# Optimization experiments

Measured on AMD Instinct MI355X. Metric: run time of the kernel, lower is better.

The kernel has to match this reference:

```python
import jax, jax.numpy as jnp
import numpy as np

N_NODES = 100000
D_EMB = 128          # per-node embedding dim; concat dim = 2*D_EMB = 256
HIDDEN = 64
N_EDGES = 300000


def setup_inputs() -> dict:
    key = jax.random.key(0)
    ks = jax.random.split(key, 8)
    src_embs = jax.random.normal(ks[0], (N_NODES, D_EMB), dtype=jnp.float32)
    dst_embs = jax.random.normal(ks[1], (N_NODES, D_EMB), dtype=jnp.float32)
    edges_src_ids = jax.random.randint(ks[2], (N_EDGES,), 0, N_NODES, dtype=jnp.int64)
    edges_dst_ids = jax.random.randint(ks[3], (N_EDGES,), 0, N_NODES, dtype=jnp.int64)
    # elayers = Linear(256, 64) -> ReLU -> Linear(64, 1)
    s1 = 1.0 / np.sqrt(2 * D_EMB)
    s2 = 1.0 / np.sqrt(HIDDEN)
    W1 = jax.random.uniform(ks[4], (2 * D_EMB, HIDDEN), jnp.float32, -s1, s1)
    b1 = jax.random.uniform(ks[5], (HIDDEN,), jnp.float32, -s1, s1)
    W2 = jax.random.uniform(ks[6], (HIDDEN, 1), jnp.float32, -s2, s2)
    b2 = jax.random.uniform(ks[7], (1,), jnp.float32, -s2, s2)
    return {
        "src_embs": src_embs,
        "dst_embs": dst_embs,
        "edges_src_ids": edges_src_ids,
        "edges_dst_ids": edges_dst_ids,
        "W1": W1,
        "b1": b1,
        "W2": W2,
        "b2": b2,
    }


def reference(src_embs, dst_embs, edges_src_ids, edges_dst_ids, W1, b1, W2, b2):
    # Gather per-edge endpoint embeddings and concatenate: [E, 2*D]
    edge_feats = jnp.concatenate(
        [src_embs[edges_src_ids], dst_embs[edges_dst_ids]], axis=1
    )
    # Linear -> ReLU -> Linear, producing one logit per edge: [E, 1]
    h = jax.nn.relu(edge_feats @ W1 + b1)
    edge_logits = h @ W2 + b2
    return edge_logits
```

## Files before the change

### kernel.cpp

```cpp
#include <hip/hip_runtime.h>
#include <hip/hip_bf16.h>

typedef float f32x4 __attribute__((ext_vector_type(4)));
typedef __bf16 bf16x8 __attribute__((ext_vector_type(8)));
typedef __bf16 bf16x4 __attribute__((ext_vector_type(4)));

#define DEMB 128
#define HIDDEN 64
#define W1T_STRIDE 264

typedef const __attribute__((address_space(1))) void* gas_ptr;
typedef __attribute__((address_space(3))) void* las_ptr;

__global__ __launch_bounds__(256) void node_part3_kernel(
    const float* __restrict__ src_embs,
    const float* __restrict__ dst_embs,
    const float* __restrict__ W1,
    __bf16* __restrict__ spart,
    __bf16* __restrict__ dpart,
    int n_tiles, int blocks_per_table)
{
    __shared__ __bf16 frag_lds[1024 * 8];
    __shared__ float  atile[4][2048];

    const int table = (blockIdx.x >= blocks_per_table) ? 1 : 0;
    const int bid = blockIdx.x - table * blocks_per_table;
    const float* __restrict__ E = table ? dst_embs : src_embs;
    __bf16* __restrict__ P = table ? dpart : spart;
    const int kofs = table * 128;

    for (int cid = threadIdx.x; cid < 1024; cid += 256) {
        const int el = cid & 15;
        const int gk = (cid >> 4) & 3;
        const int kk = (cid >> 6) & 3;
        const int t  = (cid >> 8) & 3;
        const int kbase = kofs + kk * 32 + gk * 8;
        bf16x8 ch;
#pragma unroll
        for (int j = 0; j < 8; ++j)
            ch[j] = (__bf16)W1[(kbase + j) * HIDDEN + 4 * el + t];
        *reinterpret_cast<bf16x8*>(&frag_lds[cid * 8]) = ch;
    }
    __syncthreads();

    const int lane = threadIdx.x & 63;
    const int el = lane & 15;
    const int gk = lane >> 4;
    const int wid = threadIdx.x >> 6;
    char* awc = (char*)&atile[wid][0];

    int soff[8];
#pragma unroll
    for (int op = 0; op < 8; ++op) {
        const int d = op * 1024 + lane * 16;
        soff[op] = d ^ (((d >> 9) & 7) << 4);
    }
    const int abase = (el * 512 + gk * 32) ^ ((el & 7) << 4);

    const int tstride = blocks_per_table * 4;
    for (int tile = bid * 4 + wid; tile < n_tiles; tile += tstride) {
        const char* ebase = (const char*)E + (size_t)tile * (16 * DEMB * 4);
#pragma unroll
        for (int op = 0; op < 8; ++op) {
            __builtin_amdgcn_global_load_lds(
                (gas_ptr)(ebase + soff[op]),
                (las_ptr)(awc + op * 1024), 16, 0, 0);
        }
        asm volatile("s_waitcnt vmcnt(0)" ::: "memory");

        f32x4 acc[4] = {{0.f,0.f,0.f,0.f},{0.f,0.f,0.f,0.f},
                        {0.f,0.f,0.f,0.f},{0.f,0.f,0.f,0.f}};
#pragma unroll
        for (int kk = 0; kk < 4; ++kk) {
            const int ab = abase + kk * 128;
            f32x4 lo = *reinterpret_cast<const f32x4*>(awc + ab);
            f32x4 hi = *reinterpret_cast<const f32x4*>(awc + (ab ^ 16));
            bf16x8 a;
#pragma unroll
            for (int j = 0; j < 4; ++j) { a[j] = (__bf16)lo[j]; a[4+j] = (__bf16)hi[j]; }
#pragma unroll
            for (int t = 0; t < 4; ++t) {
                const bf16x8 b = *reinterpret_cast<const bf16x8*>(
                    &frag_lds[(size_t)((t * 4 + kk) * 4 + gk) * 128 + el * 8]);
                acc[t] = __builtin_amdgcn_mfma_f32_16x16x32_bf16(a, b, acc[t], 0, 0, 0);
            }
        }

        asm volatile("" ::: "memory");
#pragma unroll
        for (int r = 0; r < 4; ++r) {
            bf16x4 pk;
#pragma unroll
            for (int t = 0; t < 4; ++t) pk[t] = (__bf16)acc[t][r];
            *reinterpret_cast<bf16x4*>(awc + (gk * 4 + r) * 128 + el * 8) = pk;
        }
        asm volatile("s_waitcnt lgkmcnt(0)" ::: "memory");
        f32x4 c0 = *reinterpret_cast<const f32x4*>(awc + lane * 32);
        f32x4 c1 = *reinterpret_cast<const f32x4*>(awc + lane * 32 + 16);
        char* pb = (char*)P + (size_t)tile * 2048;
        *reinterpret_cast<f32x4*>(pb + lane * 32) = c0;
        *reinterpret_cast<f32x4*>(pb + lane * 32 + 16) = c1;
    }
}

__global__ __launch_bounds__(256, 8) void edge_tail2_kernel(
    const __bf16* __restrict__ spart,
    const __bf16* __restrict__ dpart,
    const int* __restrict__ src_ids,
    const int* __restrict__ dst_ids,
    const float* __restrict__ b1,
    const float* __restrict__ W2,
    const float* __restrict__ b2,
    float* __restrict__ out,
    int n_edges)
{
    const int lane = threadIdx.x & 63;
    const int c = lane & 7;
    float b1v[8], w2v[8];
#pragma unroll
    for (int j = 0; j < 8; ++j) { b1v[j] = b1[c * 8 + j]; w2v[j] = W2[c * 8 + j]; }
    const float bias2 = b2[0];

    int gid = (blockIdx.x * blockDim.x + threadIdx.x) >> 3;
    const int gstride = (gridDim.x * blockDim.x) >> 3;

    for (int e = gid; e < n_edges; e += gstride) {
        const long long sid = src_ids[e];
        const long long did = dst_ids[e];
        const bf16x8 s8 = *reinterpret_cast<const bf16x8*>(spart + sid * HIDDEN + c * 8);
        const bf16x8 d8 = *reinterpret_cast<const bf16x8*>(dpart + did * HIDDEN + c * 8);
        float v = 0.f;
#pragma unroll
        for (int j = 0; j < 8; ++j) {
            float h = (float)s8[j] + (float)d8[j] + b1v[j];
            h = fmaxf(h, 0.f);
            v = fmaf(h, w2v[j], v);
        }
        v += __shfl_xor(v, 1, 64);
        v += __shfl_xor(v, 2, 64);
        v += __shfl_xor(v, 4, 64);
        if (c == 0) out[e] = v + bias2;
    }
}

__global__ __launch_bounds__(256) void edge_mlp_kernel(
    const float* __restrict__ src_embs,
    const float* __restrict__ dst_embs,
    const int* __restrict__ src_ids,
    const int* __restrict__ dst_ids,
    const float* __restrict__ W1,
    const float* __restrict__ b1,
    const float* __restrict__ W2,
    const float* __restrict__ b2,
    float* __restrict__ out,
    int n_edges, int n_groups)
{
    __shared__ __bf16 w1t[64 * W1T_STRIDE];
    for (int s = threadIdx.x; s < 256 * 64; s += 256) {
        int k = s >> 6;
        int n = s & 63;
        w1t[n * W1T_STRIDE + k] = (__bf16)W1[s];
    }
    __syncthreads();

    const int lane = threadIdx.x & 63;
    const int el = lane & 15;
    const int gk = lane >> 4;

    float b1v[4], w2v[4];
#pragma unroll
    for (int t = 0; t < 4; ++t) { b1v[t] = b1[16 * t + el]; w2v[t] = W2[16 * t + el]; }
    const float bias2 = b2[0];

    const int gw0 = blockIdx.x * 4 + (threadIdx.x >> 6);
    const int gstride = gridDim.x * 4;

    for (int g = gw0; g < n_groups; g += gstride) {
        const int e_base = g * 16;
        int e = e_base + el;
        if (e >= n_edges) e = n_edges - 1;
        const long long sid = src_ids[e];
        const long long did = dst_ids[e];
        const float* sp = src_embs + sid * DEMB + gk * 8;
        const float* dp = dst_embs + did * DEMB + gk * 8;

        f32x4 acc[4] = {{0.f,0.f,0.f,0.f},{0.f,0.f,0.f,0.f},
                        {0.f,0.f,0.f,0.f},{0.f,0.f,0.f,0.f}};
#pragma unroll
        for (int kk = 0; kk < 8; ++kk) {
            const float* ap = (kk < 4) ? (sp + kk * 32) : (dp + (kk - 4) * 32);
            f32x4 f0 = *reinterpret_cast<const f32x4*>(ap);
            f32x4 f1 = *reinterpret_cast<const f32x4*>(ap + 4);
            bf16x8 a;
#pragma unroll
            for (int j = 0; j < 4; ++j) { a[j] = (__bf16)f0[j]; a[4+j] = (__bf16)f1[j]; }
#pragma unroll
            for (int t = 0; t < 4; ++t) {
                const bf16x8 bfrag = *reinterpret_cast<const bf16x8*>(
                    &w1t[(16 * t + el) * W1T_STRIDE + kk * 32 + gk * 8]);
                acc[t] = __builtin_amdgcn_mfma_f32_16x16x32_bf16(a, bfrag, acc[t], 0, 0, 0);
            }
        }
        float s0[4];
#pragma unroll
        for (int r = 0; r < 4; ++r) {
            float v = 0.f;
#pragma unroll
            for (int t = 0; t < 4; ++t) {
                float h = acc[t][r] + b1v[t];
                h = fmaxf(h, 0.f);
                v = fmaf(h, w2v[t], v);
            }
#pragma unroll
            for (int m = 1; m < 16; m <<= 1) v += __shfl_xor(v, m, 64);
            s0[r] = v + bias2;
        }
        const int row0 = e_base + gk * 4;
        if (el == 0) {
            if (row0 + 4 <= n_edges) {
                f32x4 o = {s0[0], s0[1], s0[2], s0[3]};
                *reinterpret_cast<f32x4*>(out + row0) = o;
            } else {
#pragma unroll
                for (int r = 0; r < 4; ++r)
                    if (row0 + r < n_edges) out[row0 + r] = s0[r];
            }
        }
    }
}

extern "C" void kernel_launch(void* const* d_in, const int* in_sizes, int n_in,
                              void* d_out, int out_size, void* d_ws, size_t ws_size,
                              hipStream_t stream) {
    const float* src_embs = (const float*)d_in[0];
    const float* dst_embs = (const float*)d_in[1];
    const int*   src_ids  = (const int*)d_in[2];
    const int*   dst_ids  = (const int*)d_in[3];
    const float* W1 = (const float*)d_in[4];
    const float* b1 = (const float*)d_in[5];
    const float* W2 = (const float*)d_in[6];
    const float* b2 = (const float*)d_in[7];
    float* out = (float*)d_out;

    const int n_edges = in_sizes[2];
    const int n_nodes = in_sizes[0] / DEMB;
    const size_t part_elems = (size_t)n_nodes * HIDDEN;
    const size_t need = 2 * part_elems * sizeof(__bf16);

    if (ws_size >= need && (n_nodes % 16) == 0) {
        __bf16* spart = (__bf16*)d_ws;
        __bf16* dpart = spart + part_elems;
        const int n_tiles = n_nodes / 16;

        int bpt = 384;
        if (bpt * 4 > n_tiles) bpt = (n_tiles + 3) / 4;
        node_part3_kernel<<<2 * bpt, 256, 0, stream>>>(
            src_embs, dst_embs, W1, spart, dpart, n_tiles, bpt);

        int blocks2 = (n_edges + 31) / 32;
        if (blocks2 > 2048) blocks2 = 2048;
        edge_tail2_kernel<<<blocks2, 256, 0, stream>>>(
            spart, dpart, src_ids, dst_ids, b1, W2, b2, out, n_edges);
    } else {
        const int n_groups = (n_edges + 15) / 16;
        int blocks = (n_groups + 3) / 4;
        if (blocks > 1024) blocks = 1024;
        edge_mlp_kernel<<<blocks, 256, 0, stream>>>(
            src_embs, dst_embs, src_ids, dst_ids, W1, b1, W2, b2, out,
            n_edges, n_groups);
    }
}
```

Measured before the change: 40.37 us.

## Double-buffer node tile loads with prefetch in a 2-wave block

```diff
diff --git a/kernel.cpp b/kernel.cpp
--- a/kernel.cpp
+++ b/kernel.cpp
@@ -12,7 +12,7 @@
 typedef const __attribute__((address_space(1))) void* gas_ptr;
 typedef __attribute__((address_space(3))) void* las_ptr;
 
-__global__ __launch_bounds__(256) void node_part3_kernel(
+__global__ __launch_bounds__(128) void node_part4_kernel(
     const float* __restrict__ src_embs,
     const float* __restrict__ dst_embs,
     const float* __restrict__ W1,
@@ -21,7 +21,8 @@
     int n_tiles, int blocks_per_table)
 {
     __shared__ __bf16 frag_lds[1024 * 8];
-    __shared__ float  atile[4][2048];
+    __shared__ float  stage[2][2][2048];
+    __shared__ float  bounce[2][512];
 
     const int table = (blockIdx.x >= blocks_per_table) ? 1 : 0;
     const int bid = blockIdx.x - table * blocks_per_table;
@@ -29,7 +30,7 @@
     __bf16* __restrict__ P = table ? dpart : spart;
     const int kofs = table * 128;
 
-    for (int cid = threadIdx.x; cid < 1024; cid += 256) {
+    for (int cid = threadIdx.x; cid < 1024; cid += 128) {
         const int el = cid & 15;
         const int gk = (cid >> 4) & 3;
         const int kk = (cid >> 6) & 3;
@@ -47,7 +48,9 @@
     const int el = lane & 15;
     const int gk = lane >> 4;
     const int wid = threadIdx.x >> 6;
-    char* awc = (char*)&atile[wid][0];
+    char* buf0 = (char*)&stage[wid][0][0];
+    char* buf1 = (char*)&stage[wid][1][0];
+    char* obc  = (char*)&bounce[wid][0];
 
     int soff[8];
 #pragma unroll
@@ -57,16 +60,36 @@
     }
     const int abase = (el * 512 + gk * 32) ^ ((el & 7) << 4);
 
-    const int tstride = blocks_per_table * 4;
-    for (int tile = bid * 4 + wid; tile < n_tiles; tile += tstride) {
-        const char* ebase = (const char*)E + (size_t)tile * (16 * DEMB * 4);
-#pragma unroll
-        for (int op = 0; op < 8; ++op) {
-            __builtin_amdgcn_global_load_lds(
-                (gas_ptr)(ebase + soff[op]),
-                (las_ptr)(awc + op * 1024), 16, 0, 0);
-        }
-        asm volatile("s_waitcnt vmcnt(0)" ::: "memory");
+#define ISSUE_TILE(T, DST)                                                  \
+    do {                                                                    \
+        const char* eb_ = (const char*)E + (size_t)(T) * (16 * DEMB * 4);   \
+        _Pragma("unroll")                                                   \
+        for (int op = 0; op < 8; ++op)                                      \
+            __builtin_amdgcn_global_load_lds((gas_ptr)(eb_ + soff[op]),     \
+                                             (las_ptr)((DST) + op * 1024),  \
+                                             16, 0, 0);                     \
+    } while (0)
+
+    const int tstride = blocks_per_table * 2;
+    int tile = bid * 2 + wid;
+    int cur = 0;
+    bool have_stores = false;
+
+    if (tile < n_tiles) ISSUE_TILE(tile, buf0);
+
+    while (tile < n_tiles) {
+        const int nxt = tile + tstride;
+        const bool pf = (nxt < n_tiles);
+        char* awc = cur ? buf1 : buf0;
+        if (pf) ISSUE_TILE(nxt, cur ? buf0 : buf1);
+
+        if (pf) {
+            if (have_stores) asm volatile("s_waitcnt vmcnt(10)" ::: "memory");
+            else             asm volatile("s_waitcnt vmcnt(8)"  ::: "memory");
+        } else {
+            if (have_stores) asm volatile("s_waitcnt vmcnt(2)" ::: "memory");
+            else             asm volatile("s_waitcnt vmcnt(0)" ::: "memory");
+        }
 
         f32x4 acc[4] = {{0.f,0.f,0.f,0.f},{0.f,0.f,0.f,0.f},
                         {0.f,0.f,0.f,0.f},{0.f,0.f,0.f,0.f}};
@@ -86,21 +109,25 @@
             }
         }
 
-        asm volatile("" ::: "memory");
 #pragma unroll
         for (int r = 0; r < 4; ++r) {
             bf16x4 pk;
 #pragma unroll
             for (int t = 0; t < 4; ++t) pk[t] = (__bf16)acc[t][r];
-            *reinterpret_cast<bf16x4*>(awc + (gk * 4 + r) * 128 + el * 8) = pk;
+            *reinterpret_cast<bf16x4*>(obc + (gk * 4 + r) * 128 + el * 8) = pk;
         }
         asm volatile("s_waitcnt lgkmcnt(0)" ::: "memory");
-        f32x4 c0 = *reinterpret_cast<const f32x4*>(awc + lane * 32);
-        f32x4 c1 = *reinterpret_cast<const f32x4*>(awc + lane * 32 + 16);
+        f32x4 c0 = *reinterpret_cast<const f32x4*>(obc + lane * 32);
+        f32x4 c1 = *reinterpret_cast<const f32x4*>(obc + lane * 32 + 16);
         char* pb = (char*)P + (size_t)tile * 2048;
         *reinterpret_cast<f32x4*>(pb + lane * 32) = c0;
         *reinterpret_cast<f32x4*>(pb + lane * 32 + 16) = c1;
-    }
+
+        have_stores = true;
+        cur ^= 1;
+        tile = nxt;
+    }
+#undef ISSUE_TILE
 }
 
 __global__ __launch_bounds__(256, 8) void edge_tail2_kernel(
@@ -253,8 +280,8 @@
         const int n_tiles = n_nodes / 16;
 
         int bpt = 384;
-        if (bpt * 4 > n_tiles) bpt = (n_tiles + 3) / 4;
-        node_part3_kernel<<<2 * bpt, 256, 0, stream>>>(
+        if (bpt * 2 > n_tiles) bpt = (n_tiles + 1) / 2;
+        node_part4_kernel<<<2 * bpt, 128, 0, stream>>>(
             src_embs, dst_embs, W1, spart, dpart, n_tiles, bpt);
 
         int blocks2 = (n_edges + 31) / 32;
```

After: 42.97 us. 1.06x slower.

## Precompute W1 fragments in separate kernel and load embeddings directly to registers

Applied to the files above, without the earlier changes.

```diff
diff --git a/kernel.cpp b/kernel.cpp
--- a/kernel.cpp
+++ b/kernel.cpp
@@ -12,72 +12,82 @@
 typedef const __attribute__((address_space(1))) void* gas_ptr;
 typedef __attribute__((address_space(3))) void* las_ptr;
 
-__global__ __launch_bounds__(256) void node_part3_kernel(
+__global__ __launch_bounds__(256) void w1frag_kernel(
+    const float* __restrict__ W1, __bf16* __restrict__ wsfrag)
+{
+    const int gid = blockIdx.x * 256 + threadIdx.x;
+    if (gid >= 2048) return;
+    const int tb  = gid >> 10;
+    const int cid = gid & 1023;
+    const int el = cid & 15;
+    const int gk = (cid >> 4) & 3;
+    const int kk = (cid >> 6) & 3;
+    const int t  = (cid >> 8) & 3;
+    const int kbase = tb * 128 + kk * 32 + gk * 8;
+    bf16x8 ch;
+#pragma unroll
+    for (int j = 0; j < 8; ++j)
+        ch[j] = (__bf16)W1[(kbase + j) * HIDDEN + 4 * el + t];
+    *reinterpret_cast<bf16x8*>(wsfrag + (size_t)gid * 8) = ch;
+}
+
+__global__ __launch_bounds__(256, 6) void node_part8_kernel(
     const float* __restrict__ src_embs,
     const float* __restrict__ dst_embs,
-    const float* __restrict__ W1,
+    const __bf16* __restrict__ wsfrag,
     __bf16* __restrict__ spart,
     __bf16* __restrict__ dpart,
     int n_tiles, int blocks_per_table)
 {
     __shared__ __bf16 frag_lds[1024 * 8];
-    __shared__ float  atile[4][2048];
+    __shared__ float  bounce[4][512];
 
     const int table = (blockIdx.x >= blocks_per_table) ? 1 : 0;
     const int bid = blockIdx.x - table * blocks_per_table;
     const float* __restrict__ E = table ? dst_embs : src_embs;
     __bf16* __restrict__ P = table ? dpart : spart;
-    const int kofs = table * 128;
-
-    for (int cid = threadIdx.x; cid < 1024; cid += 256) {
-        const int el = cid & 15;
-        const int gk = (cid >> 4) & 3;
-        const int kk = (cid >> 6) & 3;
-        const int t  = (cid >> 8) & 3;
-        const int kbase = kofs + kk * 32 + gk * 8;
-        bf16x8 ch;
-#pragma unroll
-        for (int j = 0; j < 8; ++j)
-            ch[j] = (__bf16)W1[(kbase + j) * HIDDEN + 4 * el + t];
-        *reinterpret_cast<bf16x8*>(&frag_lds[cid * 8]) = ch;
-    }
-    __syncthreads();
 
     const int lane = threadIdx.x & 63;
     const int el = lane & 15;
     const int gk = lane >> 4;
     const int wid = threadIdx.x >> 6;
-    char* awc = (char*)&atile[wid][0];
-
-    int soff[8];
-#pragma unroll
-    for (int op = 0; op < 8; ++op) {
-        const int d = op * 1024 + lane * 16;
-        soff[op] = d ^ (((d >> 9) & 7) << 4);
-    }
-    const int abase = (el * 512 + gk * 32) ^ ((el & 7) << 4);
-
+
+    {
+        const char* src = (const char*)(wsfrag + (size_t)table * 1024 * 8);
+#pragma unroll
+        for (int r = 0; r < 4; ++r) {
+            const int off = (wid * 4 + r) * 1024;
+            __builtin_amdgcn_global_load_lds(
+                (gas_ptr)(src + off + lane * 16),
+                (las_ptr)((char*)frag_lds + off), 16, 0, 0);
+        }
+        asm volatile("s_waitcnt vmcnt(0)" ::: "memory");
+    }
+    __syncthreads();
+
+    char* obc = (char*)&bounce[wid][0];
     const int tstride = blocks_per_table * 4;
+
     for (int tile = bid * 4 + wid; tile < n_tiles; tile += tstride) {
-        const char* ebase = (const char*)E + (size_t)tile * (16 * DEMB * 4);
-#pragma unroll
-        for (int op = 0; op < 8; ++op) {
-            __builtin_amdgcn_global_load_lds(
-                (gas_ptr)(ebase + soff[op]),
-                (las_ptr)(awc + op * 1024), 16, 0, 0);
-        }
-        asm volatile("s_waitcnt vmcnt(0)" ::: "memory");
+        const float* rp = E + (size_t)tile * 2048 + el * 128 + gk * 8;
+
+        f32x4 R[8];
+#pragma unroll
+        for (int kk = 0; kk < 4; ++kk) {
+            R[2 * kk]     = *reinterpret_cast<const f32x4*>(rp + kk * 32);
+            R[2 * kk + 1] = *reinterpret_cast<const f32x4*>(rp + kk * 32 + 4);
+        }
 
         f32x4 acc[4] = {{0.f,0.f,0.f,0.f},{0.f,0.f,0.f,0.f},
                         {0.f,0.f,0.f,0.f},{0.f,0.f,0.f,0.f}};
 #pragma unroll
         for (int kk = 0; kk < 4; ++kk) {
-            const int ab = abase + kk * 128;
-            f32x4 lo = *reinterpret_cast<const f32x4*>(awc + ab);
-            f32x4 hi = *reinterpret_cast<const f32x4*>(awc + (ab ^ 16));
             bf16x8 a;
 #pragma unroll
-            for (int j = 0; j < 4; ++j) { a[j] = (__bf16)lo[j]; a[4+j] = (__bf16)hi[j]; }
+            for (int j = 0; j < 4; ++j) {
+                a[j]     = (__bf16)R[2 * kk][j];
+                a[4 + j] = (__bf16)R[2 * kk + 1][j];
+            }
 #pragma unroll
             for (int t = 0; t < 4; ++t) {
                 const bf16x8 b = *reinterpret_cast<const bf16x8*>(
@@ -86,17 +96,16 @@
             }
         }
 
-        asm volatile("" ::: "memory");
 #pragma unroll
         for (int r = 0; r < 4; ++r) {
             bf16x4 pk;
 #pragma unroll
             for (int t = 0; t < 4; ++t) pk[t] = (__bf16)acc[t][r];
-            *reinterpret_cast<bf16x4*>(awc + (gk * 4 + r) * 128 + el * 8) = pk;
+            *reinterpret_cast<bf16x4*>(obc + (gk * 4 + r) * 128 + el * 8) = pk;
         }
         asm volatile("s_waitcnt lgkmcnt(0)" ::: "memory");
-        f32x4 c0 = *reinterpret_cast<const f32x4*>(awc + lane * 32);
-        f32x4 c1 = *reinterpret_cast<const f32x4*>(awc + lane * 32 + 16);
+        f32x4 c0 = *reinterpret_cast<const f32x4*>(obc + lane * 32);
+        f32x4 c1 = *reinterpret_cast<const f32x4*>(obc + lane * 32 + 16);
         char* pb = (char*)P + (size_t)tile * 2048;
         *reinterpret_cast<f32x4*>(pb + lane * 32) = c0;
         *reinterpret_cast<f32x4*>(pb + lane * 32 + 16) = c1;
@@ -245,17 +254,20 @@
     const int n_edges = in_sizes[2];
     const int n_nodes = in_sizes[0] / DEMB;
     const size_t part_elems = (size_t)n_nodes * HIDDEN;
-    const size_t need = 2 * part_elems * sizeof(__bf16);
+    const size_t need = 2 * part_elems * sizeof(__bf16) + 32768;
 
     if (ws_size >= need && (n_nodes % 16) == 0) {
         __bf16* spart = (__bf16*)d_ws;
         __bf16* dpart = spart + part_elems;
+        __bf16* wsfrag = dpart + part_elems;
         const int n_tiles = n_nodes / 16;
 
-        int bpt = 384;
+        w1frag_kernel<<<8, 256, 0, stream>>>(W1, wsfrag);
+
+        int bpt = 768;
         if (bpt * 4 > n_tiles) bpt = (n_tiles + 3) / 4;
-        node_part3_kernel<<<2 * bpt, 256, 0, stream>>>(
-            src_embs, dst_embs, W1, spart, dpart, n_tiles, bpt);
+        node_part8_kernel<<<2 * bpt, 256, 0, stream>>>(
+            src_embs, dst_embs, wsfrag, spart, dpart, n_tiles, bpt);
 
         int blocks2 = (n_edges + 31) / 32;
         if (blocks2 > 2048) blocks2 = 2048;
```

Result: slower. 44.68 us (+10.7%).
